# Performance work log

Hardware: AMD Instinct MI355X
Metric: run time of the kernel (lower is better)

## Reference

```python
import jax, jax.numpy as jnp
import numpy as np

B, T, F, H = 2048, 256, 64, 128


def setup_inputs() -> dict:
    key = jax.random.key(0)
    ks = jax.random.split(key, 9)
    s = 0.1  # small init scale for stable recurrence
    return {
        "x": jax.random.normal(ks[0], (B, T, F), dtype=jnp.float32),
        "W_ih": jax.random.normal(ks[1], (4 * H, F), dtype=jnp.float32) * s,
        "W_hh": jax.random.normal(ks[2], (4 * H, H), dtype=jnp.float32) * s,
        "b_ih": jax.random.normal(ks[3], (4 * H,), dtype=jnp.float32) * s,
        "b_hh": jax.random.normal(ks[4], (4 * H,), dtype=jnp.float32) * s,
        "W1": jax.random.normal(ks[5], (32, H), dtype=jnp.float32) * s,
        "b1": jax.random.normal(ks[6], (32,), dtype=jnp.float32) * s,
        "W2": jax.random.normal(ks[7], (1, 32), dtype=jnp.float32) * s,
        "b2": jax.random.normal(ks[8], (1,), dtype=jnp.float32) * s,
    }


def reference(x, W_ih, W_hh, b_ih, b_hh, W1, b1, W2, b2):
    # Single-layer LSTM (PyTorch gate order i, f, g, o), take last hidden state.
    Bsz, Tlen, _ = x.shape
    Hdim = W_hh.shape[1]
    xt = jnp.swapaxes(x, 0, 1)  # [T, B, F]
    bias = b_ih + b_hh  # [4H]

    def step(carry, xb):
        h, c = carry
        gates = xb @ W_ih.T + h @ W_hh.T + bias  # [B, 4H]
        i, f, g, o = jnp.split(gates, 4, axis=-1)
        i = jax.nn.sigmoid(i)
        f = jax.nn.sigmoid(f)
        g = jnp.tanh(g)
        o = jax.nn.sigmoid(o)
        c = f * c + i * g
        h = o * jnp.tanh(c)
        return (h, c), None

    h0 = jnp.zeros((Bsz, Hdim), dtype=x.dtype)
    c0 = jnp.zeros((Bsz, Hdim), dtype=x.dtype)
    (h_last, _), _ = jax.lax.scan(step, (h0, c0), xt)

    # head: Linear(H,32) -> ReLU -> Linear(32,1) -> Sigmoid -> squeeze(-1)
    z = jax.nn.relu(h_last @ W1.T + b1)
    return jax.nn.sigmoid(z @ W2.T + b2)[:, 0]
```

## Files before the change

kernel.cpp:

```cpp
#include <hip/hip_runtime.h>


#define Bsz   2048
#define Tlen  256
#define Fdim  64
#define Hdim  128
#define BB    8
#define NTHREADS 512
#define TILE_E 512
#define NKT   6
#define BUF_E (NKT * TILE_E)

using bf16x8 = __attribute__((ext_vector_type(8))) __bf16;
using f32x4  = __attribute__((ext_vector_type(4))) float;

__device__ __forceinline__ float fast_rcp(float x) {
#if __has_builtin(__builtin_amdgcn_rcpf)
    return __builtin_amdgcn_rcpf(x);
#else
    return 1.0f / x;
#endif
}
__device__ __forceinline__ float fast_exp2(float x) {
#if __has_builtin(__builtin_amdgcn_exp2f)
    return __builtin_amdgcn_exp2f(x);
#else
    return exp2f(x);
#endif
}
__device__ __forceinline__ float fsig(float x) {
    return fast_rcp(1.0f + fast_exp2(-1.4426950408889634f * x));
}
__device__ __forceinline__ float ftanh(float x) {
    float e = fast_exp2(-2.8853900817779268f * x);
    return (1.0f - e) * fast_rcp(1.0f + e);
}

__global__ __launch_bounds__(NTHREADS, 2)
void lstm_fused(const float* __restrict__ x,
                const float* __restrict__ W_ih,
                const float* __restrict__ W_hh,
                const float* __restrict__ b_ih,
                const float* __restrict__ b_hh,
                const float* __restrict__ W1,
                const float* __restrict__ b1,
                const float* __restrict__ W2,
                const float* __restrict__ b2,
                float* __restrict__ out)
{
    __shared__ __bf16 Abuf[2][BUF_E];
    __shared__ float  hlast[BB * Hdim];
    __shared__ float  zbuf[BB * 32];

    const int tid  = threadIdx.x;
    const int w    = tid >> 6;
    const int lane = tid & 63;
    const int quad = lane >> 4;
    const int l16  = lane & 15;
    const int b0   = blockIdx.x * BB;

    bf16x8 bw[NKT][4];
    #pragma unroll
    for (int kt = 0; kt < NKT; ++kt) {
        const int k0 = kt * 32 + quad * 8;
        #pragma unroll
        for (int g = 0; g < 4; ++g) {
            const int n = g * Hdim + w * 16 + l16;
            const float* p = (kt < 2) ? (W_ih + (size_t)n * Fdim + k0)
                                      : (W_hh + (size_t)n * Hdim + (k0 - Fdim));
            float4 lo = *(const float4*)p;
            float4 hi = *(const float4*)(p + 4);
            bf16x8 r;
            r[0]=(__bf16)lo.x; r[1]=(__bf16)lo.y; r[2]=(__bf16)lo.z; r[3]=(__bf16)lo.w;
            r[4]=(__bf16)hi.x; r[5]=(__bf16)hi.y; r[6]=(__bf16)hi.z; r[7]=(__bf16)hi.w;
            bw[kt][g] = r;
        }
    }
    float biasv[4];
    #pragma unroll
    for (int g = 0; g < 4; ++g) {
        const int n = g * Hdim + w * 16 + l16;
        biasv[g] = b_ih[n] + b_hh[n];
    }

    const bool sx_on  = tid < 256;
    const int  sx_row = tid & 7;
    const int  sx_fp  = (tid >> 3) & 31;
    const float* xrp  = x + (size_t)(b0 + sx_row) * (Tlen * Fdim) + 2 * sx_fp;
    const int sx_elem = (sx_fp >> 4) * TILE_E
                      + ((((sx_fp >> 2) & 3) * 16 + sx_row) * 8) + 2 * (sx_fp & 3);

    const int er0 = (quad < 2) ? quad * 4 : (quad - 2) * 4 + 2;
    const int hc  = w * 16 + l16;
    const int hw_elem = (2 + (hc >> 5)) * TILE_E
                      + ((((hc >> 3) & 3) * 16 + er0) * 8) + (hc & 7);

    for (int i = tid; i < 2 * BUF_E; i += NTHREADS)
        ((__bf16*)Abuf)[i] = (__bf16)0.0f;
    float2 xpre = make_float2(0.f, 0.f);
    if (sx_on) xpre = *(const float2*)xrp;
    __syncthreads();
    if (sx_on) {
        Abuf[0][sx_elem]     = (__bf16)xpre.x;
        Abuf[0][sx_elem + 1] = (__bf16)xpre.y;
        xpre = *(const float2*)(xrp + Fdim);
    }
    __syncthreads();

    float cc0 = 0.f, cc1 = 0.f;

    #pragma unroll 2
    for (int t = 0; t < Tlen; ++t) {
        const int p = t & 1;
        const __bf16* rb   = Abuf[p];
        __bf16*       wbuf = (__bf16*)Abuf[1 - p];

        bf16x8 af[NKT];
        #pragma unroll
        for (int kt = 0; kt < NKT; ++kt)
            af[kt] = *(const bf16x8*)&rb[kt * TILE_E + lane * 8];

        float2 xnext = make_float2(0.f, 0.f);
        if (sx_on && (t + 2) < Tlen)
            xnext = *(const float2*)(xrp + (size_t)(t + 2) * Fdim);

        f32x4 acc[4];
        #pragma unroll
        for (int g = 0; g < 4; ++g)
            acc[g] = (f32x4){biasv[g], biasv[g], biasv[g], biasv[g]};
        #pragma unroll
        for (int kt = 0; kt < NKT; ++kt) {
            #pragma unroll
            for (int g = 0; g < 4; ++g)
                acc[g] = __builtin_amdgcn_mfma_f32_16x16x32_bf16(af[kt], bw[kt][g], acc[g], 0, 0, 0);
        }

        float ga[4][2];
        #pragma unroll
        for (int g = 0; g < 4; ++g) {
            float s2 = __shfl_xor(acc[g][2], 32);
            float s3 = __shfl_xor(acc[g][3], 32);
            ga[g][0] = (quad < 2) ? acc[g][0] : s2;
            ga[g][1] = (quad < 2) ? acc[g][1] : s3;
        }

        #pragma unroll
        for (int s = 0; s < 2; ++s) {
            float iv = fsig(ga[0][s]);
            float fv = fsig(ga[1][s]);
            float gv = ftanh(ga[2][s]);
            float ov = fsig(ga[3][s]);
            float c  = fv * (s ? cc1 : cc0) + iv * gv;
            if (s) cc1 = c; else cc0 = c;
            float h  = ov * ftanh(c);
            wbuf[hw_elem + 8 * s] = (__bf16)h;
            if (t == Tlen - 1) hlast[(er0 + s) * Hdim + hc] = h;
        }

        if (sx_on && (t + 1) < Tlen) {
            wbuf[sx_elem]     = (__bf16)xpre.x;
            wbuf[sx_elem + 1] = (__bf16)xpre.y;
        }
        xpre = xnext;
        __syncthreads();
    }

    if (tid < 256) {
        const int b = tid >> 5, n = tid & 31;
        const float4* w4 = (const float4*)(W1 + n * Hdim);
        const float4* h4 = (const float4*)(hlast + b * Hdim);
        float s = b1[n];
        #pragma unroll
        for (int kk = 0; kk < Hdim / 4; ++kk) {
            float4 wv = w4[kk];
            float4 hv = h4[kk];
            s += wv.x * hv.x + wv.y * hv.y + wv.z * hv.z + wv.w * hv.w;
        }
        zbuf[b * 32 + n] = fmaxf(s, 0.0f);
    }
    __syncthreads();
    if (tid < 8) {
        float s = b2[0];
        #pragma unroll
        for (int n = 0; n < 32; ++n) s += zbuf[tid * 32 + n] * W2[n];
        out[b0 + tid] = fsig(s);
    }
}

extern "C" void kernel_launch(void* const* d_in, const int* in_sizes, int n_in,
                              void* d_out, int out_size, void* d_ws, size_t ws_size,
                              hipStream_t stream) {
    const float* x    = (const float*)d_in[0];
    const float* W_ih = (const float*)d_in[1];
    const float* W_hh = (const float*)d_in[2];
    const float* b_ih = (const float*)d_in[3];
    const float* b_hh = (const float*)d_in[4];
    const float* W1   = (const float*)d_in[5];
    const float* b1   = (const float*)d_in[6];
    const float* W2   = (const float*)d_in[7];
    const float* b2   = (const float*)d_in[8];
    float* out = (float*)d_out;

    dim3 grid(Bsz / BB), block(NTHREADS);
    lstm_fused<<<grid, block, 0, stream>>>(x, W_ih, W_hh, b_ih, b_hh, W1, b1, W2, b2, out);
}
```

Baseline: 409.0 us.

## Halve batch rows per block to double grid and raise occupancy

Each workgroup now handles 4 batch rows instead of 8, which doubles the grid to 512 blocks. Launch bounds change to allow 4 blocks per CU. Each lane now computes a single hidden element per step: the gate values are gathered with a full shuffle, the second cell-state register is dropped, and bf16 pairs are written as packed 32-bit stores. The aim is more parallel blocks hiding the serial per-step latency, at the cost of MFMA tiles that are mostly zero padding and register pressure under the tighter launch bound.

```diff
diff --git a/kernel.cpp b/kernel.cpp
--- a/kernel.cpp
+++ b/kernel.cpp
@@ -5,8 +5,8 @@
 #define Tlen  256
 #define Fdim  64
 #define Hdim  128
-#define BB    8
-#define NTHREADS 512
+#define ROWS  4
+#define NTH   512
 #define TILE_E 512
 #define NKT   6
 #define BUF_E (NKT * TILE_E)
@@ -36,7 +36,11 @@
     return (1.0f - e) * fast_rcp(1.0f + e);
 }
 
-__global__ __launch_bounds__(NTHREADS, 2)
+__device__ __forceinline__ int frag_elem(int row, int k) {
+    return (k >> 5) * TILE_E + ((((k >> 3) & 3) * 16 + row) * 8) + (k & 7);
+}
+
+__global__ __launch_bounds__(NTH, 4)
 void lstm_fused(const float* __restrict__ x,
                 const float* __restrict__ W_ih,
                 const float* __restrict__ W_hh,
@@ -49,15 +53,15 @@
                 float* __restrict__ out)
 {
     __shared__ __bf16 Abuf[2][BUF_E];
-    __shared__ float  hlast[BB * Hdim];
-    __shared__ float  zbuf[BB * 32];
+    __shared__ float  hlast[ROWS * Hdim];
+    __shared__ float  zbuf[ROWS * 32];
 
     const int tid  = threadIdx.x;
     const int w    = tid >> 6;
     const int lane = tid & 63;
     const int quad = lane >> 4;
     const int l16  = lane & 15;
-    const int b0   = blockIdx.x * BB;
+    const int b0   = blockIdx.x * ROWS;
 
     bf16x8 bw[NKT][4];
     #pragma unroll
@@ -83,37 +87,36 @@
         biasv[g] = b_ih[n] + b_hh[n];
     }
 
-    const bool sx_on  = tid < 256;
-    const int  sx_row = tid & 7;
-    const int  sx_fp  = (tid >> 3) & 31;
-    const float* xrp  = x + (size_t)(b0 + sx_row) * (Tlen * Fdim) + 2 * sx_fp;
-    const int sx_elem = (sx_fp >> 4) * TILE_E
-                      + ((((sx_fp >> 2) & 3) * 16 + sx_row) * 8) + 2 * (sx_fp & 3);
-
-    const int er0 = (quad < 2) ? quad * 4 : (quad - 2) * 4 + 2;
-    const int hc  = w * 16 + l16;
-    const int hw_elem = (2 + (hc >> 5)) * TILE_E
-                      + ((((hc >> 3) & 3) * 16 + er0) * 8) + (hc & 7);
-
-    for (int i = tid; i < 2 * BUF_E; i += NTHREADS)
-        ((__bf16*)Abuf)[i] = (__bf16)0.0f;
+    const bool sx_on  = tid < 128;
+    const int  sx_row = (tid >> 5) & 3;
+    const int  sx_fp  = tid & 31;
+    const int  f0     = 2 * sx_fp;
+    const float* xrp  = x + (size_t)(b0 + sx_row) * (Tlen * Fdim) + f0;
+    const int sx_elem = frag_elem(sx_row, f0);
+
+    const int hc     = 16 * w + l16;
+    const int h_elem = frag_elem(quad, Fdim + hc);
+
+    {
+        const int r_ = tid >> 7;
+        const int hk = tid & 127;
+        Abuf[0][frag_elem(r_, Fdim + hk)] = (__bf16)0.0f;
+    }
     float2 xpre = make_float2(0.f, 0.f);
-    if (sx_on) xpre = *(const float2*)xrp;
+    if (sx_on) {
+        float2 v0 = *(const float2*)xrp;
+        __bf16 a0[2] = {(__bf16)v0.x, (__bf16)v0.y};
+        *(uint*)&Abuf[0][sx_elem] = *(uint*)a0;
+        xpre = *(const float2*)(xrp + Fdim);
+    }
     __syncthreads();
-    if (sx_on) {
-        Abuf[0][sx_elem]     = (__bf16)xpre.x;
-        Abuf[0][sx_elem + 1] = (__bf16)xpre.y;
-        xpre = *(const float2*)(xrp + Fdim);
-    }
-    __syncthreads();
-
-    float cc0 = 0.f, cc1 = 0.f;
-
-    #pragma unroll 2
+
+    float cst = 0.0f;
+
     for (int t = 0; t < Tlen; ++t) {
         const int p = t & 1;
-        const __bf16* rb   = Abuf[p];
-        __bf16*       wbuf = (__bf16*)Abuf[1 - p];
+        const __bf16* rb = Abuf[p];
+        __bf16*      wbf = (__bf16*)Abuf[1 - p];
 
         bf16x8 af[NKT];
         #pragma unroll
@@ -135,37 +138,38 @@
                 acc[g] = __builtin_amdgcn_mfma_f32_16x16x32_bf16(af[kt], bw[kt][g], acc[g], 0, 0, 0);
         }
 
-        float ga[4][2];
+        float ga[4];
         #pragma unroll
         for (int g = 0; g < 4; ++g) {
-            float s2 = __shfl_xor(acc[g][2], 32);
-            float s3 = __shfl_xor(acc[g][3], 32);
-            ga[g][0] = (quad < 2) ? acc[g][0] : s2;
-            ga[g][1] = (quad < 2) ? acc[g][1] : s3;
-        }
-
-        #pragma unroll
-        for (int s = 0; s < 2; ++s) {
-            float iv = fsig(ga[0][s]);
-            float fv = fsig(ga[1][s]);
-            float gv = ftanh(ga[2][s]);
-            float ov = fsig(ga[3][s]);
-            float c  = fv * (s ? cc1 : cc0) + iv * gv;
-            if (s) cc1 = c; else cc0 = c;
-            float h  = ov * ftanh(c);
-            wbuf[hw_elem + 8 * s] = (__bf16)h;
-            if (t == Tlen - 1) hlast[(er0 + s) * Hdim + hc] = h;
+            float t0 = __shfl(acc[g][0], l16);
+            float t1 = __shfl(acc[g][1], l16);
+            float t2 = __shfl(acc[g][2], l16);
+            float t3 = __shfl(acc[g][3], l16);
+            float s01 = (quad & 1) ? t1 : t0;
+            float s23 = (quad & 1) ? t3 : t2;
+            ga[g] = (quad & 2) ? s23 : s01;
+        }
+
+        {
+            float iv = fsig(ga[0]);
+            float fv = fsig(ga[1]);
+            float gv = ftanh(ga[2]);
+            float ov = fsig(ga[3]);
+            cst = fv * cst + iv * gv;
+            float h = ov * ftanh(cst);
+            wbf[h_elem] = (__bf16)h;
+            if (t == Tlen - 1) hlast[quad * Hdim + hc] = h;
         }
 
         if (sx_on && (t + 1) < Tlen) {
-            wbuf[sx_elem]     = (__bf16)xpre.x;
-            wbuf[sx_elem + 1] = (__bf16)xpre.y;
+            __bf16 xa[2] = {(__bf16)xpre.x, (__bf16)xpre.y};
+            *(uint*)&wbf[sx_elem] = *(uint*)xa;
         }
         xpre = xnext;
         __syncthreads();
     }
 
-    if (tid < 256) {
+    if (tid < ROWS * 32) {
         const int b = tid >> 5, n = tid & 31;
         const float4* w4 = (const float4*)(W1 + n * Hdim);
         const float4* h4 = (const float4*)(hlast + b * Hdim);
@@ -179,7 +183,7 @@
         zbuf[b * 32 + n] = fmaxf(s, 0.0f);
     }
     __syncthreads();
-    if (tid < 8) {
+    if (tid < ROWS) {
         float s = b2[0];
         #pragma unroll
         for (int n = 0; n < 32; ++n) s += zbuf[tid * 32 + n] * W2[n];
@@ -201,6 +205,6 @@
     const float* b2   = (const float*)d_in[8];
     float* out = (float*)d_out;
 
-    dim3 grid(Bsz / BB), block(NTHREADS);
+    dim3 grid(Bsz / ROWS), block(NTH);
     lstm_fused<<<grid, block, 0, stream>>>(x, W_ih, W_hh, b_ih, b_hh, W1, b1, W2, b2, out);
 }
```

After: 1.463 ms. 3.58x slower.
